# Optimization experiments

Hardware: AMD Instinct MI355X
Metric: run time of the kernel (lower is better)

Reference implementation:

```python
import jax, jax.numpy as jnp
import numpy as np

N_NODES = 10000
N_EDGES = 80000
N_GRAPHS = 64
H, D = 4, 512          # num_heads, out_feats
EMB = 768
HFEAT = 512
NCLS = 2
SLOPE = 0.2            # DGL GATConv default negative_slope
BN_EPS = 1e-5


def setup_inputs() -> dict:
    key = jax.random.key(0)
    ks = jax.random.split(key, 24)
    f32 = jnp.float32
    rn = lambda k, s, sc=0.02: jax.random.normal(k, s, dtype=f32) * sc
    inp = {
        "node_feat": jax.random.normal(ks[0], (N_NODES, EMB), dtype=f32),
        "func_feat": jax.random.normal(ks[1], (N_NODES, EMB), dtype=f32),
        "W1": rn(ks[2], (EMB, H * D)),
        "al1": rn(ks[3], (H, D), 0.1),
        "ar1": rn(ks[4], (H, D), 0.1),
        "b1": jnp.zeros((H * D,), f32),
        "W2": rn(ks[5], (H * D, H * D)),
        "al2": rn(ks[6], (H, D), 0.1),
        "ar2": rn(ks[7], (H, D), 0.1),
        "b2": jnp.zeros((H * D,), f32),
        "Wfc": rn(ks[8], (H * D, HFEAT)),
        "bfc": jnp.zeros((HFEAT,), f32),
        "Wfco": rn(ks[9], (EMB, HFEAT)),
        "bfco": jnp.zeros((HFEAT,), f32),
        "Wh": rn(ks[10], (8, HFEAT, HFEAT)),
        "bh": jnp.zeros((8, HFEAT), f32),
        "gamma": jnp.ones((HFEAT,), f32),
        "beta": jnp.zeros((HFEAT,), f32),
        "Whfc": rn(ks[11], (HFEAT, HFEAT)),
        "bhfc": jnp.zeros((HFEAT,), f32),
        "Wf": rn(ks[12], (HFEAT, NCLS)),
        "bf": jnp.zeros((NCLS,), f32),
        "src": jax.random.randint(ks[13], (N_EDGES,), 0, N_NODES),
        "dst": jax.random.randint(ks[14], (N_EDGES,), 0, N_NODES),
        "graph_id": jnp.sort(jax.random.randint(ks[15], (N_NODES,), 0, N_GRAPHS)),
    }
    return inp


def gat_conv(h, W, al, ar, b, src, dst):
    """DGL GATConv (eval mode): fc -> per-head attention logits -> edge
    softmax over incoming edges -> scatter-sum -> +bias. Returns (N, H*D)."""
    feat = (h @ W).reshape(-1, H, D)                      # (N,H,D)
    el = jnp.einsum('nhd,hd->nh', feat, al)               # (N,H)
    er = jnp.einsum('nhd,hd->nh', feat, ar)
    e = jax.nn.leaky_relu(el[src] + er[dst], SLOPE)       # (E,H)
    emax = jax.ops.segment_max(e, dst, num_segments=N_NODES)
    ex = jnp.exp(e - emax[dst])
    den = jax.ops.segment_sum(ex, dst, num_segments=N_NODES)
    a = ex / den[dst]                                     # edge softmax (E,H)
    msg = feat[src] * a[:, :, None]                       # (E,H,D) gather+weight
    out = jax.ops.segment_sum(msg, dst, num_segments=N_NODES)
    return (out + b.reshape(1, H, D)).reshape(-1, H * D)


def reference(node_feat, func_feat, W1, al1, ar1, b1, W2, al2, ar2, b2,
              Wfc, bfc, Wfco, bfco, Wh, bh, gamma, beta, Whfc, bhfc,
              Wf, bf, src, dst, graph_id):
    h = gat_conv(node_feat, W1, al1, ar1, b1, src, dst)   # (N, 2048)
    h = gat_conv(h, W2, al2, ar2, b2, src, dst)           # (N, 2048)
    h = jax.nn.elu(h @ Wfc + bfc)                         # (N, 512)
    h_func = jax.nn.elu(func_feat @ Wfco + bfco)          # (N, 512)
    for i in range(8):
        h = jax.nn.elu(h @ Wh[i] + bh[i])
        h_func = jax.nn.elu(h_func @ Wh[i] + bh[i])       # dead for output (as in torch)
    counts = jax.ops.segment_sum(jnp.ones((N_NODES,), h.dtype), graph_id,
                                 num_segments=N_GRAPHS)
    hg = jax.ops.segment_sum(h, graph_id, num_segments=N_GRAPHS)
    hg = hg / jnp.maximum(counts, 1.0)[:, None]           # dgl.mean_nodes (G, 512)
    # BatchNorm1d eval with running_mean=0, running_var=1
    hg = hg / jnp.sqrt(1.0 + BN_EPS) * gamma + beta
    hg = jax.nn.elu(hg @ Whfc + bhfc)
    return hg @ Wf + bf                                   # (G, NCLS)
```

## Files before the change

kernel.cpp:

```cpp
#include <hip/hip_runtime.h>
#include <hip/hip_bf16.h>
#include <math.h>

#define N_NODES 10000
#define N_EDGES 80000
#define N_GRAPHS 64
#define NH 4
#define HD 512
#define HDTOT 2048
#define EMB 768
#define HFEAT 512

typedef _Float16 half8 __attribute__((ext_vector_type(8)));
typedef _Float16 half4 __attribute__((ext_vector_type(4)));
typedef float f32x4 __attribute__((ext_vector_type(4)));

__device__ __forceinline__ void gload_lds16(const void* g, void* l) {
  __builtin_amdgcn_global_load_lds(
      (const __attribute__((address_space(1))) unsigned int*)g,
      (__attribute__((address_space(3))) unsigned int*)l, 16, 0, 0);
}

template <int BM>
__global__ __launch_bounds__(256) void gemm_f16_kernel(
    const _Float16* __restrict__ A, const _Float16* __restrict__ BT,
    const float* __restrict__ bias, _Float16* __restrict__ C,
    int M, int N, int K, int act) {
  constexpr int WR = (BM == 128) ? 2 : 1;
  constexpr int WC = 4 / WR;
  constexpr int MI = (BM / WR) / 16;
  constexpr int NI = (128 / WC) / 16;
  constexpr int NW = NI * 16;
  constexpr int CS = NW + 4;
  constexpr int GPR = NW / 8;

  __shared__ _Float16 smem[(BM + 128) * 64];
  _Float16* As = smem;
  _Float16* Bs = smem + BM * 64;

  const int bn = blockIdx.x * 128, bm = blockIdx.y * BM;
  const int t = threadIdx.x;
  const int lane = t & 63, wave = t >> 6;
  const int wr = wave / WC, wc = wave % WC;
  const int m0 = wr * (BM / WR), n0 = wc * NW;
  const int fr = lane & 15, fq = lane >> 4;

  f32x4 acc[MI][NI];
#pragma unroll
  for (int i = 0; i < MI; ++i)
#pragma unroll
    for (int j = 0; j < NI; ++j) acc[i][j] = (f32x4){0.f, 0.f, 0.f, 0.f};

  for (int k0 = 0; k0 < K; k0 += 64) {
    __syncthreads();
#pragma unroll
    for (int it = 0; it < BM / 32; ++it) {
      int gid = it * 256 + t;
      int r = gid >> 3;
      int q = (gid & 7) ^ (r & 7);
      int grow = bm + r;
      if (grow >= M) grow = M - 1;
      gload_lds16(A + (size_t)grow * K + k0 + q * 8,
                  &As[(it * 256 + wave * 64) * 8]);
    }
#pragma unroll
    for (int it = 0; it < 4; ++it) {
      int gid = it * 256 + t;
      int r = gid >> 3;
      int q = (gid & 7) ^ (r & 7);
      gload_lds16(BT + (size_t)(bn + r) * K + k0 + q * 8,
                  &Bs[(it * 256 + wave * 64) * 8]);
    }
    __syncthreads();

#pragma unroll
    for (int kk = 0; kk < 2; ++kk) {
      half8 af[MI], bf[NI];
#pragma unroll
      for (int mi = 0; mi < MI; ++mi) {
        int m = m0 + mi * 16 + fr;
        af[mi] = *(const half8*)&As[m * 64 + (((kk * 4 + fq) ^ (m & 7))) * 8];
      }
#pragma unroll
      for (int ni = 0; ni < NI; ++ni) {
        int n = n0 + ni * 16 + fr;
        bf[ni] = *(const half8*)&Bs[n * 64 + (((kk * 4 + fq) ^ (n & 7))) * 8];
      }
#pragma unroll
      for (int mi = 0; mi < MI; ++mi)
#pragma unroll
        for (int ni = 0; ni < NI; ++ni)
          acc[mi][ni] = __builtin_amdgcn_mfma_f32_16x16x32_f16(
              af[mi], bf[ni], acc[mi][ni], 0, 0, 0);
    }
  }
  __syncthreads();
  _Float16* cs = smem + wave * 16 * CS;
#pragma unroll
  for (int mi = 0; mi < MI; ++mi) {
#pragma unroll
    for (int ni = 0; ni < NI; ++ni) {
      float bb = bias ? bias[bn + n0 + ni * 16 + fr] : 0.f;
#pragma unroll
      for (int j = 0; j < 4; ++j) {
        float v = acc[mi][ni][j] + bb;
        if (act == 1) v = v > 0.f ? v : expm1f(v);
        cs[(fq * 4 + j) * CS + ni * 16 + fr] = (_Float16)v;
      }
    }
#pragma unroll
    for (int i = 0; i < NW / 32; ++i) {
      int piece = i * 64 + lane;
      int r = piece / GPR, g = piece % GPR;
      int grow = bm + m0 + mi * 16 + r;
      if (grow < M) {
        half8 v = *(const half8*)&cs[r * CS + g * 8];
        *(half8*)&C[(size_t)grow * N + bn + n0 + g * 8] = v;
      }
    }
  }
}

__global__ __launch_bounds__(256) void convert_wt_kernel(
    const float* __restrict__ W, _Float16* __restrict__ WT, int K, int N) {
  __shared__ float tile[32][33];
  W += (size_t)blockIdx.z * K * N;
  WT += (size_t)blockIdx.z * K * N;
  int k0 = blockIdx.x * 32, n0 = blockIdx.y * 32;
  int t = threadIdx.x;
  int r = t >> 3, c4 = (t & 7) * 4;
  float4 v = *(const float4*)(W + (size_t)(k0 + r) * N + n0 + c4);
  tile[r][c4 + 0] = v.x;
  tile[r][c4 + 1] = v.y;
  tile[r][c4 + 2] = v.z;
  tile[r][c4 + 3] = v.w;
  __syncthreads();
  float x0 = tile[c4 + 0][r], x1 = tile[c4 + 1][r];
  float x2 = tile[c4 + 2][r], x3 = tile[c4 + 3][r];
  size_t o = (size_t)(n0 + r) * K + k0 + c4;
  *(half4*)&WT[o] = (half4){(_Float16)x0, (_Float16)x1, (_Float16)x2, (_Float16)x3};
}

__global__ void convert_f32_f16_kernel(const float* __restrict__ x,
                                       _Float16* __restrict__ y, int n4) {
  int gid = blockIdx.x * blockDim.x + threadIdx.x;
  if (gid >= n4) return;
  float4 v = *(const float4*)(x + gid * 4);
  *(half4*)(y + gid * 4) =
      (half4){(_Float16)v.x, (_Float16)v.y, (_Float16)v.z, (_Float16)v.w};
}

__global__ void hist_kernel(const int* __restrict__ dst, int* __restrict__ cnt, int E) {
  int gid = blockIdx.x * blockDim.x + threadIdx.x;
  if (gid < E) atomicAdd(&cnt[dst[gid]], 1);
}

__global__ void scan_kernel(const int* __restrict__ cnt, int* __restrict__ row_ptr,
                            int* __restrict__ cursor, int n) {
  __shared__ int part[256];
  int t = threadIdx.x;
  int chunk = (n + 255) / 256;
  int s0 = t * chunk;
  int s1 = min(s0 + chunk, n);
  int sum = 0;
  for (int i = s0; i < s1; ++i) sum += cnt[i];
  part[t] = sum;
  __syncthreads();
  if (t == 0) {
    int acc = 0;
    for (int i = 0; i < 256; ++i) { int v = part[i]; part[i] = acc; acc += v; }
    row_ptr[n] = acc;
  }
  __syncthreads();
  int run = part[t];
  for (int i = s0; i < s1; ++i) {
    row_ptr[i] = run;
    cursor[i] = run;
    run += cnt[i];
  }
}

__global__ void scatter_kernel(const int* __restrict__ src, const int* __restrict__ dst,
                               int* __restrict__ cursor, int* __restrict__ csr_src,
                               int E) {
  int gid = blockIdx.x * blockDim.x + threadIdx.x;
  if (gid < E) {
    int d = dst[gid];
    int pos = atomicAdd(&cursor[d], 1);
    csr_src[pos] = src[gid];
  }
}

__global__ __launch_bounds__(256) void el_er_kernel(
    const _Float16* __restrict__ feat, const float* __restrict__ al,
    const float* __restrict__ ar, float* __restrict__ el, float* __restrict__ er) {
  int n = blockIdx.x;
  int t = threadIdx.x;
  int h = t >> 6, lane = t & 63;
  half8 f = *(const half8*)(feat + (size_t)n * HDTOT + h * HD + lane * 8);
  const float* ap = al + h * HD + lane * 8;
  const float* rp = ar + h * HD + lane * 8;
  float4 a0 = *(const float4*)ap, a1 = *(const float4*)(ap + 4);
  float4 r0 = *(const float4*)rp, r1 = *(const float4*)(rp + 4);
  float f0 = (float)f[0], f1 = (float)f[1], f2 = (float)f[2], f3 = (float)f[3];
  float f4 = (float)f[4], f5 = (float)f[5], f6 = (float)f[6], f7 = (float)f[7];
  float sl = f0 * a0.x + f1 * a0.y + f2 * a0.z + f3 * a0.w +
             f4 * a1.x + f5 * a1.y + f6 * a1.z + f7 * a1.w;
  float sr = f0 * r0.x + f1 * r0.y + f2 * r0.z + f3 * r0.w +
             f4 * r1.x + f5 * r1.y + f6 * r1.z + f7 * r1.w;
  for (int off = 32; off; off >>= 1) {
    sl += __shfl_down(sl, off);
    sr += __shfl_down(sr, off);
  }
  if (lane == 0) {
    el[n * NH + h] = sl;
    er[n * NH + h] = sr;
  }
}

__global__ __launch_bounds__(256) void edge_softmax_kernel(
    const float* __restrict__ el, const float* __restrict__ er,
    const int* __restrict__ csr_src, const int* __restrict__ row_ptr,
    float* __restrict__ e_buf) {
  int n = blockIdx.x;
  int t = threadIdx.x;
  int h = t >> 6, lane = t & 63;
  int s = row_ptr[n], epos = row_ptr[n + 1];
  if (s == epos) return;
  float ern = er[n * NH + h];
  float m = -INFINITY;
  for (int p = s + lane; p < epos; p += 64) {
    float v = el[csr_src[p] * NH + h] + ern;
    v = v >= 0.f ? v : 0.2f * v;
    e_buf[p * NH + h] = v;
    m = fmaxf(m, v);
  }
  for (int off = 32; off; off >>= 1) m = fmaxf(m, __shfl_xor(m, off));
  float sum = 0.f;
  for (int p = s + lane; p < epos; p += 64) {
    float ex = expf(e_buf[p * NH + h] - m);
    e_buf[p * NH + h] = ex;
    sum += ex;
  }
  for (int off = 32; off; off >>= 1) sum += __shfl_xor(sum, off);
  float inv = 1.f / sum;
  for (int p = s + lane; p < epos; p += 64) e_buf[p * NH + h] *= inv;
}

__global__ __launch_bounds__(256) void aggregate_kernel(
    const _Float16* __restrict__ feat, const float* __restrict__ e_buf,
    const int* __restrict__ row_ptr, const int* __restrict__ csr_src,
    const float* __restrict__ bias, _Float16* __restrict__ out) {
  int n = blockIdx.x;
  int t = threadIdx.x;
  int base = t * 8;
  int h = t >> 6;
  float acc[8] = {0.f, 0.f, 0.f, 0.f, 0.f, 0.f, 0.f, 0.f};
  int s = row_ptr[n], epos = row_ptr[n + 1];
  int p = s;
  for (; p + 4 <= epos; p += 4) {
    int sn0 = csr_src[p + 0], sn1 = csr_src[p + 1];
    int sn2 = csr_src[p + 2], sn3 = csr_src[p + 3];
    float a0 = e_buf[(p + 0) * NH + h];
    float a1 = e_buf[(p + 1) * NH + h];
    float a2 = e_buf[(p + 2) * NH + h];
    float a3 = e_buf[(p + 3) * NH + h];
    half8 f0 = *(const half8*)(feat + (size_t)sn0 * HDTOT + base);
    half8 f1 = *(const half8*)(feat + (size_t)sn1 * HDTOT + base);
    half8 f2 = *(const half8*)(feat + (size_t)sn2 * HDTOT + base);
    half8 f3 = *(const half8*)(feat + (size_t)sn3 * HDTOT + base);
#pragma unroll
    for (int i = 0; i < 8; ++i)
      acc[i] += a0 * (float)f0[i] + a1 * (float)f1[i] +
                a2 * (float)f2[i] + a3 * (float)f3[i];
  }
  for (; p < epos; ++p) {
    int sn = csr_src[p];
    float a = e_buf[p * NH + h];
    half8 f = *(const half8*)(feat + (size_t)sn * HDTOT + base);
#pragma unroll
    for (int i = 0; i < 8; ++i) acc[i] += a * (float)f[i];
  }
  float4 b0 = *(const float4*)(bias + base);
  float4 b1 = *(const float4*)(bias + base + 4);
  half8 o;
  o[0] = (_Float16)(acc[0] + b0.x); o[1] = (_Float16)(acc[1] + b0.y);
  o[2] = (_Float16)(acc[2] + b0.z); o[3] = (_Float16)(acc[3] + b0.w);
  o[4] = (_Float16)(acc[4] + b1.x); o[5] = (_Float16)(acc[5] + b1.y);
  o[6] = (_Float16)(acc[6] + b1.z); o[7] = (_Float16)(acc[7] + b1.w);
  *(half8*)(out + (size_t)n * HDTOT + base) = o;
}

__global__ __launch_bounds__(512) void pool_kernel(
    const _Float16* __restrict__ h, const int* __restrict__ graph_id,
    float* __restrict__ hg, float* __restrict__ counts) {
  int g = blockIdx.x;
  __shared__ int s_lo, s_hi;
  if (threadIdx.x == 0) {
    int lo = 0, hi = N_NODES;
    while (lo < hi) { int m = (lo + hi) >> 1; if (graph_id[m] < g) lo = m + 1; else hi = m; }
    s_lo = lo;
    int lo2 = lo, hi2 = N_NODES;
    while (lo2 < hi2) { int m = (lo2 + hi2) >> 1; if (graph_id[m] < g + 1) lo2 = m + 1; else hi2 = m; }
    s_hi = lo2;
  }
  __syncthreads();
  int lo = s_lo, hi = s_hi;
  int col = threadIdx.x;
  float acc = 0.f;
  for (int n = lo; n < hi; ++n) acc += (float)h[(size_t)n * HFEAT + col];
  hg[g * HFEAT + col] = acc;
  if (col == 0) counts[g] = (float)(hi - lo);
}

__global__ __launch_bounds__(256) void final_kernel(
    const float* __restrict__ hg, const float* __restrict__ counts,
    const float* __restrict__ gamma, const float* __restrict__ beta,
    const float* __restrict__ Whfc, const float* __restrict__ bhfc,
    const float* __restrict__ Wf, const float* __restrict__ bf,
    float* __restrict__ out) {
  __shared__ float sh[HFEAT];
  __shared__ float st[HFEAT];
  __shared__ float r0[4], r1[4];
  int g = blockIdx.x, t = threadIdx.x;
  float invc = 1.f / fmaxf(counts[g], 1.f);
  float bnscale = rsqrtf(1.f + 1e-5f);
  for (int j = t; j < HFEAT; j += 256) {
    float v = hg[g * HFEAT + j] * invc;
    sh[j] = v * bnscale * gamma[j] + beta[j];
  }
  __syncthreads();
  for (int j = t; j < HFEAT; j += 256) {
    float acc = bhfc[j];
    for (int k = 0; k < HFEAT; ++k) acc += sh[k] * Whfc[k * HFEAT + j];
    st[j] = acc > 0.f ? acc : expm1f(acc);
  }
  __syncthreads();
  float p0 = 0.f, p1 = 0.f;
  for (int j = t; j < HFEAT; j += 256) {
    p0 += st[j] * Wf[j * 2 + 0];
    p1 += st[j] * Wf[j * 2 + 1];
  }
  for (int off = 32; off; off >>= 1) {
    p0 += __shfl_down(p0, off);
    p1 += __shfl_down(p1, off);
  }
  int w = t >> 6;
  if ((t & 63) == 0) { r0[w] = p0; r1[w] = p1; }
  __syncthreads();
  if (t == 0) {
    out[g * 2 + 0] = r0[0] + r0[1] + r0[2] + r0[3] + bf[0];
    out[g * 2 + 1] = r1[0] + r1[1] + r1[2] + r1[3] + bf[1];
  }
}

static void gemm_raw(const _Float16* A, const _Float16* wt, const float* bias,
                     _Float16* C, int M, int N, int K, int act,
                     bool small_m_tile, hipStream_t stream) {
  if (small_m_tile) {
    dim3 grid(N / 128, (M + 63) / 64);
    hipLaunchKernelGGL(gemm_f16_kernel<64>, grid, dim3(256), 0, stream,
                       A, wt, bias, C, M, N, K, act);
  } else {
    dim3 grid(N / 128, (M + 127) / 128);
    hipLaunchKernelGGL(gemm_f16_kernel<128>, grid, dim3(256), 0, stream,
                       A, wt, bias, C, M, N, K, act);
  }
}

static void gemm(const _Float16* A, const float* W, _Float16* wt,
                 const float* bias, _Float16* C, int M, int N, int K, int act,
                 bool small_m_tile, hipStream_t stream) {
  hipLaunchKernelGGL(convert_wt_kernel, dim3(K / 32, N / 32, 1), dim3(256),
                     0, stream, W, wt, K, N);
  gemm_raw(A, wt, bias, C, M, N, K, act, small_m_tile, stream);
}

static void gat_layer(const _Float16* h_in, int K_in, const float* W, _Float16* wt,
                      const float* al, const float* ar, const float* b,
                      const int* row_ptr, const int* csr_src,
                      _Float16* featbuf, float* el, float* er,
                      float* e_buf, _Float16* out, hipStream_t stream) {
  gemm(h_in, W, wt, nullptr, featbuf, N_NODES, HDTOT, K_in, 0, false, stream);
  hipLaunchKernelGGL(el_er_kernel, dim3(N_NODES), dim3(256), 0, stream, featbuf, al, ar, el, er);
  hipLaunchKernelGGL(edge_softmax_kernel, dim3(N_NODES), dim3(256), 0, stream,
                     el, er, csr_src, row_ptr, e_buf);
  hipLaunchKernelGGL(aggregate_kernel, dim3(N_NODES), dim3(256), 0, stream,
                     featbuf, e_buf, row_ptr, csr_src, b, out);
}

extern "C" void kernel_launch(void* const* d_in, const int* in_sizes, int n_in,
                              void* d_out, int out_size, void* d_ws, size_t ws_size,
                              hipStream_t stream) {
  const float* node_feat = (const float*)d_in[0];
  const float* W1 = (const float*)d_in[2];
  const float* al1 = (const float*)d_in[3];
  const float* ar1 = (const float*)d_in[4];
  const float* b1 = (const float*)d_in[5];
  const float* W2 = (const float*)d_in[6];
  const float* al2 = (const float*)d_in[7];
  const float* ar2 = (const float*)d_in[8];
  const float* b2 = (const float*)d_in[9];
  const float* Wfc = (const float*)d_in[10];
  const float* bfc = (const float*)d_in[11];
  const float* Wh = (const float*)d_in[14];
  const float* bh = (const float*)d_in[15];
  const float* gamma = (const float*)d_in[16];
  const float* beta = (const float*)d_in[17];
  const float* Whfc = (const float*)d_in[18];
  const float* bhfc = (const float*)d_in[19];
  const float* Wf = (const float*)d_in[20];
  const float* bf = (const float*)d_in[21];
  const int* src = (const int*)d_in[22];
  const int* dst = (const int*)d_in[23];
  const int* graph_id = (const int*)d_in[24];
  float* out = (float*)d_out;

  _Float16* P0 = (_Float16*)d_ws;
  _Float16* P1 = P0 + (size_t)N_NODES * HDTOT;
  _Float16* Pin = P1 + (size_t)N_NODES * HDTOT;
  _Float16* wt = Pin + (size_t)N_NODES * EMB;
  _Float16* whh = wt + (size_t)2048 * 2048;
  float* el = (float*)(whh + (size_t)8 * HFEAT * HFEAT);
  float* er = el + N_NODES * NH;
  float* e_buf = er + N_NODES * NH;
  float* hg = e_buf + (size_t)N_EDGES * NH;
  float* counts = hg + N_GRAPHS * HFEAT;
  int* cnt = (int*)(counts + N_GRAPHS);
  int* row_ptr = cnt + N_NODES;
  int* cursor = row_ptr + N_NODES + 1;
  int* csr_src = cursor + N_NODES;

  hipMemsetAsync(cnt, 0, N_NODES * sizeof(int), stream);
  hipLaunchKernelGGL(hist_kernel, dim3((N_EDGES + 255) / 256), dim3(256), 0, stream,
                     dst, cnt, N_EDGES);
  hipLaunchKernelGGL(scan_kernel, dim3(1), dim3(256), 0, stream, cnt, row_ptr, cursor, N_NODES);
  hipLaunchKernelGGL(scatter_kernel, dim3((N_EDGES + 255) / 256), dim3(256), 0, stream,
                     src, dst, cursor, csr_src, N_EDGES);

  int n4 = N_NODES * EMB / 4;
  hipLaunchKernelGGL(convert_f32_f16_kernel, dim3((n4 + 255) / 256), dim3(256), 0, stream,
                     node_feat, Pin, n4);
  hipLaunchKernelGGL(convert_wt_kernel, dim3(HFEAT / 32, HFEAT / 32, 8),
                     dim3(256), 0, stream, Wh, whh, HFEAT, HFEAT);

  gat_layer(Pin, EMB, W1, wt, al1, ar1, b1, row_ptr, csr_src,
            P0, el, er, e_buf, P1, stream);
  gat_layer(P1, HDTOT, W2, wt, al2, ar2, b2, row_ptr, csr_src,
            P0, el, er, e_buf, P1, stream);

  gemm(P1, Wfc, wt, bfc, P0, N_NODES, HFEAT, HDTOT, 1, true, stream);

  _Float16* cur = P0;
  _Float16* nxt = P1;
  for (int i = 0; i < 8; ++i) {
    gemm_raw(cur, whh + (size_t)i * HFEAT * HFEAT, bh + (size_t)i * HFEAT, nxt,
             N_NODES, HFEAT, HFEAT, 1, true, stream);
    _Float16* tmp = cur; cur = nxt; nxt = tmp;
  }

  hipLaunchKernelGGL(pool_kernel, dim3(N_GRAPHS), dim3(512), 0, stream,
                     cur, graph_id, hg, counts);

  hipLaunchKernelGGL(final_kernel, dim3(N_GRAPHS), dim3(256), 0, stream,
                     hg, counts, gamma, beta, Whfc, bhfc, Wf, bf, out);
}
```

Before: 763.6 us.

## Fuse attention logit dot products into GEMM epilogue and single-pass small-degree softmax

Computes the per-node, per-head el/er attention logits inside the feature GEMM epilogue. Each wave reduces its accumulator tiles against al/ar with shuffles, combines them through shared-memory atomics, then adds into the global el/er buffers with atomics. This removes the separate el_er kernel and its re-read of the feature matrix, at the cost of an extra memset and atomic contention. The memset clears 2*N*NH floats from el, which assumes er sits right after el in the workspace. Edge softmax also gets a register-only path for nodes with degree up to 64, avoiding repeated e_buf round trips.

```diff
diff --git a/kernel.cpp b/kernel.cpp
--- a/kernel.cpp
+++ b/kernel.cpp
@@ -25,7 +25,9 @@
 __global__ __launch_bounds__(256) void gemm_f16_kernel(
     const _Float16* __restrict__ A, const _Float16* __restrict__ BT,
     const float* __restrict__ bias, _Float16* __restrict__ C,
-    int M, int N, int K, int act) {
+    int M, int N, int K, int act,
+    const float* __restrict__ al, const float* __restrict__ ar,
+    float* __restrict__ el_g, float* __restrict__ er_g) {
   constexpr int WR = (BM == 128) ? 2 : 1;
   constexpr int WC = 4 / WR;
   constexpr int MI = (BM / WR) / 16;
@@ -35,6 +37,7 @@
   constexpr int GPR = NW / 8;
 
   __shared__ _Float16 smem[(BM + 128) * 64];
+  __shared__ float elp[BM], erp[BM];
   _Float16* As = smem;
   _Float16* Bs = smem + BM * 64;
 
@@ -95,7 +98,18 @@
     }
   }
   __syncthreads();
+  if (el_g && t < BM) { elp[t] = 0.f; erp[t] = 0.f; }
+  if (el_g) __syncthreads();
+
   _Float16* cs = smem + wave * 16 * CS;
+  float av[NI], rv[NI];
+  if (el_g) {
+#pragma unroll
+    for (int ni = 0; ni < NI; ++ni) {
+      av[ni] = al[bn + n0 + ni * 16 + fr];
+      rv[ni] = ar[bn + n0 + ni * 16 + fr];
+    }
+  }
 #pragma unroll
   for (int mi = 0; mi < MI; ++mi) {
 #pragma unroll
@@ -106,6 +120,27 @@
         float v = acc[mi][ni][j] + bb;
         if (act == 1) v = v > 0.f ? v : expm1f(v);
         cs[(fq * 4 + j) * CS + ni * 16 + fr] = (_Float16)v;
+      }
+    }
+    if (el_g) {
+#pragma unroll
+      for (int j = 0; j < 4; ++j) {
+        float pe = 0.f, pr = 0.f;
+#pragma unroll
+        for (int ni = 0; ni < NI; ++ni) {
+          pe += acc[mi][ni][j] * av[ni];
+          pr += acc[mi][ni][j] * rv[ni];
+        }
+#pragma unroll
+        for (int off = 1; off < 16; off <<= 1) {
+          pe += __shfl_xor(pe, off);
+          pr += __shfl_xor(pr, off);
+        }
+        if (fr == 0) {
+          int lrow = m0 + mi * 16 + fq * 4 + j;
+          atomicAdd(&elp[lrow], pe);
+          atomicAdd(&erp[lrow], pr);
+        }
       }
     }
 #pragma unroll
@@ -117,6 +152,14 @@
         half8 v = *(const half8*)&cs[r * CS + g * 8];
         *(half8*)&C[(size_t)grow * N + bn + n0 + g * 8] = v;
       }
+    }
+  }
+  if (el_g) {
+    __syncthreads();
+    int h = bn >> 9;
+    if (t < BM && bm + t < M) {
+      atomicAdd(&el_g[(bm + t) * NH + h], elp[t]);
+      atomicAdd(&er_g[(bm + t) * NH + h], erp[t]);
     }
   }
 }
@@ -191,33 +234,6 @@
   }
 }
 
-__global__ __launch_bounds__(256) void el_er_kernel(
-    const _Float16* __restrict__ feat, const float* __restrict__ al,
-    const float* __restrict__ ar, float* __restrict__ el, float* __restrict__ er) {
-  int n = blockIdx.x;
-  int t = threadIdx.x;
-  int h = t >> 6, lane = t & 63;
-  half8 f = *(const half8*)(feat + (size_t)n * HDTOT + h * HD + lane * 8);
-  const float* ap = al + h * HD + lane * 8;
-  const float* rp = ar + h * HD + lane * 8;
-  float4 a0 = *(const float4*)ap, a1 = *(const float4*)(ap + 4);
-  float4 r0 = *(const float4*)rp, r1 = *(const float4*)(rp + 4);
-  float f0 = (float)f[0], f1 = (float)f[1], f2 = (float)f[2], f3 = (float)f[3];
-  float f4 = (float)f[4], f5 = (float)f[5], f6 = (float)f[6], f7 = (float)f[7];
-  float sl = f0 * a0.x + f1 * a0.y + f2 * a0.z + f3 * a0.w +
-             f4 * a1.x + f5 * a1.y + f6 * a1.z + f7 * a1.w;
-  float sr = f0 * r0.x + f1 * r0.y + f2 * r0.z + f3 * r0.w +
-             f4 * r1.x + f5 * r1.y + f6 * r1.z + f7 * r1.w;
-  for (int off = 32; off; off >>= 1) {
-    sl += __shfl_down(sl, off);
-    sr += __shfl_down(sr, off);
-  }
-  if (lane == 0) {
-    el[n * NH + h] = sl;
-    er[n * NH + h] = sr;
-  }
-}
-
 __global__ __launch_bounds__(256) void edge_softmax_kernel(
     const float* __restrict__ el, const float* __restrict__ er,
     const int* __restrict__ csr_src, const int* __restrict__ row_ptr,
@@ -226,8 +242,29 @@
   int t = threadIdx.x;
   int h = t >> 6, lane = t & 63;
   int s = row_ptr[n], epos = row_ptr[n + 1];
-  if (s == epos) return;
+  int deg = epos - s;
+  if (deg == 0) return;
   float ern = er[n * NH + h];
+  if (deg <= 64) {
+    int p = s + lane;
+    bool on = lane < deg;
+    float logit = 0.f;
+    float m = -INFINITY;
+    if (on) {
+      float v = el[csr_src[p] * NH + h] + ern;
+      logit = v >= 0.f ? v : 0.2f * v;
+      m = logit;
+    }
+#pragma unroll
+    for (int off = 32; off; off >>= 1) m = fmaxf(m, __shfl_xor(m, off));
+    float ex = on ? expf(logit - m) : 0.f;
+    float sum = ex;
+#pragma unroll
+    for (int off = 32; off; off >>= 1) sum += __shfl_xor(sum, off);
+    float inv = 1.f / sum;
+    if (on) e_buf[p * NH + h] = ex * inv;
+    return;
+  }
   float m = -INFINITY;
   for (int p = s + lane; p < epos; p += 64) {
     float v = el[csr_src[p] * NH + h] + ern;
@@ -356,24 +393,28 @@
 
 static void gemm_raw(const _Float16* A, const _Float16* wt, const float* bias,
                      _Float16* C, int M, int N, int K, int act,
-                     bool small_m_tile, hipStream_t stream) {
+                     bool small_m_tile, hipStream_t stream,
+                     const float* al = nullptr, const float* ar = nullptr,
+                     float* el = nullptr, float* er = nullptr) {
   if (small_m_tile) {
     dim3 grid(N / 128, (M + 63) / 64);
     hipLaunchKernelGGL(gemm_f16_kernel<64>, grid, dim3(256), 0, stream,
-                       A, wt, bias, C, M, N, K, act);
+                       A, wt, bias, C, M, N, K, act, al, ar, el, er);
   } else {
     dim3 grid(N / 128, (M + 127) / 128);
     hipLaunchKernelGGL(gemm_f16_kernel<128>, grid, dim3(256), 0, stream,
-                       A, wt, bias, C, M, N, K, act);
+                       A, wt, bias, C, M, N, K, act, al, ar, el, er);
   }
 }
 
 static void gemm(const _Float16* A, const float* W, _Float16* wt,
                  const float* bias, _Float16* C, int M, int N, int K, int act,
-                 bool small_m_tile, hipStream_t stream) {
+                 bool small_m_tile, hipStream_t stream,
+                 const float* al = nullptr, const float* ar = nullptr,
+                 float* el = nullptr, float* er = nullptr) {
   hipLaunchKernelGGL(convert_wt_kernel, dim3(K / 32, N / 32, 1), dim3(256),
                      0, stream, W, wt, K, N);
-  gemm_raw(A, wt, bias, C, M, N, K, act, small_m_tile, stream);
+  gemm_raw(A, wt, bias, C, M, N, K, act, small_m_tile, stream, al, ar, el, er);
 }
 
 static void gat_layer(const _Float16* h_in, int K_in, const float* W, _Float16* wt,
@@ -381,8 +422,9 @@
                       const int* row_ptr, const int* csr_src,
                       _Float16* featbuf, float* el, float* er,
                       float* e_buf, _Float16* out, hipStream_t stream) {
-  gemm(h_in, W, wt, nullptr, featbuf, N_NODES, HDTOT, K_in, 0, false, stream);
-  hipLaunchKernelGGL(el_er_kernel, dim3(N_NODES), dim3(256), 0, stream, featbuf, al, ar, el, er);
+  hipMemsetAsync(el, 0, 2 * N_NODES * NH * sizeof(float), stream);
+  gemm(h_in, W, wt, nullptr, featbuf, N_NODES, HDTOT, K_in, 0, false, stream,
+       al, ar, el, er);
   hipLaunchKernelGGL(edge_softmax_kernel, dim3(N_NODES), dim3(256), 0, stream,
                      el, er, csr_src, row_ptr, e_buf);
   hipLaunchKernelGGL(aggregate_kernel, dim3(N_NODES), dim3(256), 0, stream,
```

Result: slower. 791.6 us (+3.7%).
